# Optimization experiments

Hardware: AMD Instinct MI355X
Metric: run time of the kernel (lower is better)

The kernel has to match this reference:

```python
import jax, jax.numpy as jnp
import numpy as np

N = 100000
E = 1600000
IN_FEATS = 256
OUT_FEATS = 128
THRESHOLD = 0.5


def setup_inputs() -> dict:
    key = jax.random.key(0)
    k1, k2, k3, k4, k5, k6, k7 = jax.random.split(key, 7)
    return {
        "feat": jax.random.normal(k1, (N, IN_FEATS), dtype=jnp.float32),
        "src": jax.random.randint(k2, (E,), 0, N, dtype=jnp.int32),
        "dst": jax.random.randint(k3, (E,), 0, N, dtype=jnp.int32),
        "edge_weight": jax.random.uniform(k4, (E,), dtype=jnp.float32),
        "weight": jax.random.normal(k5, (IN_FEATS, OUT_FEATS), dtype=jnp.float32),
        "bias": jax.random.normal(k6, (OUT_FEATS,), dtype=jnp.float32),
        "mask_real": jax.random.uniform(k7, (IN_FEATS, OUT_FEATS), dtype=jnp.float32),
    }


def reference(feat, src, dst, edge_weight, weight, bias, mask_real):
    ones_e = jnp.ones((E,), dtype=feat.dtype)
    # norm == 'both': scale source feats by out_degree^-0.5 (clamped at 1)
    out_deg = jnp.clip(jax.ops.segment_sum(ones_e, src, num_segments=N), 1.0)
    feat_src = feat * (out_deg ** -0.5)[:, None]  # [N, IN]
    # binarized mask with straight-through estimator (training-mode path)
    hard = (mask_real > THRESHOLD).astype(mask_real.dtype)
    mask_t = jax.lax.stop_gradient(hard - mask_real) + mask_real
    w = mask_t * weight  # [IN, OUT]
    # in_feats > out_feats: project before aggregation
    feat_src = feat_src @ w  # [N, OUT]
    # u_mul_e then sum: gather source feats, scale by edge weight, scatter-add to dst
    msgs = feat_src[src] * edge_weight[:, None]  # [E, OUT]
    rst = jax.ops.segment_sum(msgs, dst, num_segments=N)  # [N, OUT]
    # norm == 'both': scale by in_degree^-0.5 (clamped at 1)
    in_deg = jnp.clip(jax.ops.segment_sum(ones_e, dst, num_segments=N), 1.0)
    rst = rst * (in_deg ** -0.5)[:, None]
    return rst + bias
```

## Files before the change

### kernel.cpp

```cpp
#include <hip/hip_runtime.h>

#define N_NODES 100000
#define N_EDGES 1600000
#define IN_F 256
#define OUT_F 128
#define NBUCK 391
#define NPART 256
#define CHUNK (N_EDGES / NPART)
#define BCAP 5632

#define ODBLK 256
#define ODCHUNK (N_EDGES / ODBLK)
#define ODW 25000

typedef __attribute__((ext_vector_type(8))) short short8;
typedef __attribute__((ext_vector_type(4))) float f32x4;

__device__ __forceinline__ unsigned bf16_rne(float f) {
    unsigned u = __float_as_uint(f);
    return (u + 0x7fffu + ((u >> 16) & 1u)) >> 16;
}

__global__ void mask_w_kernel(const float* __restrict__ weight,
                              const float* __restrict__ mask_real,
                              unsigned short* __restrict__ wmT) {
    int i = blockIdx.x * blockDim.x + threadIdx.x;
    if (i < IN_F * OUT_F) {
        int k = i >> 7;
        int n = i & 127;
        float v = (mask_real[i] > 0.5f) ? weight[i] : 0.0f;
        wmT[(size_t)n * IN_F + k] = (unsigned short)bf16_rne(v);
    }
}

__global__ __launch_bounds__(256) void outdeg_part_kernel(const int* __restrict__ src,
                                                          unsigned* __restrict__ part) {
    __shared__ unsigned h[ODW];
    int b = blockIdx.x, t = threadIdx.x;
    for (int i = t; i < ODW; i += 256) h[i] = 0u;
    __syncthreads();
    int base = b * ODCHUNK;
    for (int i = t; i < ODCHUNK; i += 256) {
        unsigned s = (unsigned)src[base + i];
        atomicAdd(&h[s >> 2], 1u << ((s & 3u) * 8u));
    }
    __syncthreads();
    unsigned* op = part + (size_t)b * ODW;
    for (int i = t; i < ODW; i += 256) op[i] = h[i];
}

__global__ __launch_bounds__(256) void outdeg_reduce_kernel(const unsigned* __restrict__ part,
                                                            unsigned* __restrict__ outpk) {
    int d = blockIdx.x * 256 + threadIdx.x;
    if (d < ODW) {
        unsigned sum = 0u;
#pragma unroll 8
        for (int b = 0; b < ODBLK; b++) sum += part[(size_t)b * ODW + d];
        outpk[d] = sum;
    }
}

__global__ __launch_bounds__(256) void hist_kernel(const int* __restrict__ dst,
                                                   unsigned* __restrict__ hist) {
    __shared__ unsigned h[NBUCK];
    int p = blockIdx.x, t = threadIdx.x;
    for (int b = t; b < NBUCK; b += 256) h[b] = 0u;
    __syncthreads();
    int base = p * CHUNK;
    for (int i = t; i < CHUNK; i += 256)
        atomicAdd(&h[(unsigned)dst[base + i] >> 8], 1u);
    __syncthreads();
    for (int b = t; b < NBUCK; b += 256)
        hist[(size_t)p * NBUCK + b] = h[b];
}

__global__ __launch_bounds__(256) void scan_reduce_hist(const unsigned* __restrict__ hist,
                                                        unsigned* __restrict__ bsum) {
    __shared__ unsigned red[256];
    int b = blockIdx.x, t = threadIdx.x;
    red[t] = hist[(size_t)t * NBUCK + b];
    __syncthreads();
#pragma unroll
    for (int d = 128; d > 0; d >>= 1) {
        if (t < d) red[t] += red[t + d];
        __syncthreads();
    }
    if (t == 0) bsum[b] = red[0];
}

__global__ __launch_bounds__(512) void scan_spine(const unsigned* __restrict__ bsum,
                                                  unsigned* __restrict__ bpref) {
    __shared__ unsigned part[512];
    int t = threadIdx.x;
    unsigned v = (t < NBUCK) ? bsum[t] : 0u;
    part[t] = v;
    __syncthreads();
#pragma unroll
    for (int d = 1; d < 512; d <<= 1) {
        unsigned x = (t >= d) ? part[t - d] : 0u;
        __syncthreads();
        part[t] += x;
        __syncthreads();
    }
    if (t < NBUCK) bpref[t] = part[t] - v;
}

__global__ __launch_bounds__(256) void scan_apply_hist(const unsigned* __restrict__ hist,
                                                       const unsigned* __restrict__ bpref,
                                                       unsigned* __restrict__ scanned) {
    __shared__ unsigned part[256];
    int b = blockIdx.x, t = threadIdx.x;
    unsigned v = hist[(size_t)t * NBUCK + b];
    part[t] = v;
    __syncthreads();
#pragma unroll
    for (int d = 1; d < 256; d <<= 1) {
        unsigned x = (t >= d) ? part[t - d] : 0u;
        __syncthreads();
        part[t] += x;
        __syncthreads();
    }
    scanned[(size_t)b * 256 + t] = bpref[b] + part[t] - v;
}

__global__ __launch_bounds__(256) void scatter_kernel(const int* __restrict__ src,
                                                      const int* __restrict__ dst,
                                                      const float* __restrict__ ew,
                                                      const unsigned* __restrict__ scanned,
                                                      uint2* __restrict__ tmp) {
    __shared__ unsigned cur[NBUCK];
    int p = blockIdx.x, t = threadIdx.x;
    for (int b = t; b < NBUCK; b += 256) cur[b] = scanned[(size_t)b * 256 + p];
    __syncthreads();
    int base = p * CHUNK;
    for (int i = t; i < CHUNK; i += 256) {
        int e = base + i;
        int s = src[e];
        int d = dst[e];
        unsigned pos = atomicAdd(&cur[(unsigned)d >> 8], 1u);
        tmp[pos] = make_uint2((unsigned)s | (((unsigned)d & 255u) << 17),
                              __float_as_uint(ew[e]));
    }
}

__global__ __launch_bounds__(256) void fillB_kernel(const uint2* __restrict__ tmp,
                                                    const unsigned* __restrict__ scanned,
                                                    unsigned* __restrict__ offsets,
                                                    uint2* __restrict__ smeta) {
    __shared__ uint2 ebuf[BCAP];
    __shared__ unsigned hcnt[256];
    __shared__ unsigned pref[256];
    int b = blockIdx.x, t = threadIdx.x;
    unsigned base = scanned[(size_t)b * 256];
    unsigned next = (b == NBUCK - 1) ? (unsigned)N_EDGES : scanned[(size_t)(b + 1) * 256];
    int cnt = (int)(next - base);
    if (cnt > BCAP) cnt = BCAP;
    hcnt[t] = 0u;
    for (int i = t; i < cnt; i += 256) ebuf[i] = tmp[base + i];
    __syncthreads();
    for (int i = t; i < cnt; i += 256) atomicAdd(&hcnt[ebuf[i].x >> 17], 1u);
    __syncthreads();
    unsigned v = hcnt[t];
    pref[t] = v;
    __syncthreads();
#pragma unroll
    for (int d = 1; d < 256; d <<= 1) {
        unsigned x = (t >= d) ? pref[t - d] : 0u;
        __syncthreads();
        pref[t] += x;
        __syncthreads();
    }
    unsigned excl = pref[t] - v;
    int node = b * 256 + t;
    if (node <= N_NODES) offsets[node] = base + excl;
    hcnt[t] = base + excl;
    __syncthreads();
    for (int i = t; i < cnt; i += 256) {
        uint2 m = ebuf[i];
        unsigned pos = atomicAdd(&hcnt[m.x >> 17], 1u);
        smeta[pos] = make_uint2(m.x & 0x1FFFFu, m.y);
    }
}

__global__ __launch_bounds__(256) void gemm_kernel(const float* __restrict__ feat,
                                                   const unsigned short* __restrict__ wmT,
                                                   const unsigned char* __restrict__ outdeg8,
                                                   unsigned short* __restrict__ hb) {
    __shared__ unsigned short sA[64][32];
    __shared__ unsigned short sB[128][40];
    int t = threadIdx.x;
    int row0 = blockIdx.x * 64;
    int lane = t & 63, wv = t >> 6;
    int m16 = lane & 15, quad = lane >> 4;

    f32x4 acc[8];
#pragma unroll
    for (int i = 0; i < 8; i++) acc[i] = (f32x4){0.f, 0.f, 0.f, 0.f};

    int ar = t >> 2;
    int ac = (t & 3) * 8;
    int arow = min(row0 + ar, N_NODES - 1);
    const float* fptr = feat + (size_t)arow * IN_F + ac;
    int bn = t >> 2;
    int bs = (t & 3) * 8;

    for (int k0 = 0; k0 < IN_F; k0 += 32) {
        float4 v0 = *(const float4*)(fptr + k0);
        float4 v1 = *(const float4*)(fptr + k0 + 4);
        uint4 bw0 = *(const uint4*)&wmT[(size_t)bn * IN_F + k0 + bs];
        uint4 bw1 = *(const uint4*)&wmT[(size_t)(bn + 64) * IN_F + k0 + bs];
        uint4 pk;
        pk.x = bf16_rne(v0.x) | (bf16_rne(v0.y) << 16);
        pk.y = bf16_rne(v0.z) | (bf16_rne(v0.w) << 16);
        pk.z = bf16_rne(v1.x) | (bf16_rne(v1.y) << 16);
        pk.w = bf16_rne(v1.z) | (bf16_rne(v1.w) << 16);
        __syncthreads();
        *(uint4*)&sA[ar][ac] = pk;
        *(uint4*)&sB[bn][bs] = bw0;
        *(uint4*)&sB[bn + 64][bs] = bw1;
        __syncthreads();
        short8 a = *(const short8*)&sA[wv * 16 + m16][quad * 8];
#pragma unroll
        for (int nt = 0; nt < 8; nt++) {
            short8 b = *(const short8*)&sB[nt * 16 + m16][quad * 8];
            acc[nt] = __builtin_amdgcn_mfma_f32_16x16x32_bf16(a, b, acc[nt], 0, 0, 0);
        }
    }
#pragma unroll
    for (int reg = 0; reg < 4; reg++) {
        int row = row0 + wv * 16 + quad * 4 + reg;
        if (row < N_NODES) {
            float s = rsqrtf(fmaxf((float)outdeg8[row], 1.0f));
#pragma unroll
            for (int nt = 0; nt < 8; nt++)
                hb[(size_t)row * OUT_F + nt * 16 + m16] =
                    (unsigned short)bf16_rne(acc[nt][reg] * s);
        }
    }
}

__global__ __launch_bounds__(256) void gather_kernel(const uint2* __restrict__ smeta,
                                                     const unsigned* __restrict__ offsets,
                                                     const uint4* __restrict__ hrows4,
                                                     const float* __restrict__ bias,
                                                     float* __restrict__ out) {
    int lane = threadIdx.x & 63;
    int n = blockIdx.x * 4 + (threadIdx.x >> 6);
    int g = lane >> 4;
    int q = lane & 15;
    unsigned beg = offsets[n], end = offsets[n + 1];
    int deg = (int)(end - beg);

    float acc[8];
#pragma unroll
    for (int i = 0; i < 8; i++) acc[i] = 0.0f;

    for (int base = 0; base < deg; base += 64) {
        int c = min(64, deg - base);
        unsigned sv = 0u;
        float wv = 0.0f;
        if (lane < c) {
            uint2 m = smeta[beg + base + lane];
            sv = m.x;
            wv = __uint_as_float(m.y);
        }
        int nch = (c + 3) >> 2;
#pragma unroll 4
        for (int j = 0; j < nch; j++) {
            int ei = (j << 2) + g;
            unsigned s = __shfl(sv, ei);
            float w = __shfl(wv, ei);
            uint4 h = hrows4[(size_t)s * 16u + q];
            acc[0] = fmaf(__uint_as_float(h.x << 16), w, acc[0]);
            acc[1] = fmaf(__uint_as_float(h.x & 0xffff0000u), w, acc[1]);
            acc[2] = fmaf(__uint_as_float(h.y << 16), w, acc[2]);
            acc[3] = fmaf(__uint_as_float(h.y & 0xffff0000u), w, acc[3]);
            acc[4] = fmaf(__uint_as_float(h.z << 16), w, acc[4]);
            acc[5] = fmaf(__uint_as_float(h.z & 0xffff0000u), w, acc[5]);
            acc[6] = fmaf(__uint_as_float(h.w << 16), w, acc[6]);
            acc[7] = fmaf(__uint_as_float(h.w & 0xffff0000u), w, acc[7]);
        }
    }

#pragma unroll
    for (int i = 0; i < 8; i++) {
        acc[i] += __shfl_xor(acc[i], 16);
        acc[i] += __shfl_xor(acc[i], 32);
    }

    float o0, o1;
    if (g == 0)      { o0 = acc[0]; o1 = acc[1]; }
    else if (g == 1) { o0 = acc[2]; o1 = acc[3]; }
    else if (g == 2) { o0 = acc[4]; o1 = acc[5]; }
    else             { o0 = acc[6]; o1 = acc[7]; }

    float sc = rsqrtf(fmaxf((float)deg, 1.0f));
    int col = q * 8 + g * 2;
    float2 b = *(const float2*)&bias[col];
    float2 o = make_float2(o0 * sc + b.x, o1 * sc + b.y);
    *(float2*)&out[(size_t)n * OUT_F + col] = o;
}

extern "C" void kernel_launch(void* const* d_in, const int* in_sizes, int n_in,
                              void* d_out, int out_size, void* d_ws, size_t ws_size,
                              hipStream_t stream) {
    const float* feat      = (const float*)d_in[0];
    const int*   src       = (const int*)d_in[1];
    const int*   dst       = (const int*)d_in[2];
    const float* ew        = (const float*)d_in[3];
    const float* weight    = (const float*)d_in[4];
    const float* bias      = (const float*)d_in[5];
    const float* mask_real = (const float*)d_in[6];
    float* out = (float*)d_out;

    char* ws = (char*)d_ws;
    size_t o = 0;
    auto take = [&](size_t bytes) {
        char* p = ws + o;
        o = (o + bytes + 255) & ~(size_t)255;
        return p;
    };
    unsigned short* wmT     = (unsigned short*)take((size_t)IN_F * OUT_F * 2);
    unsigned*       outpk   = (unsigned*)take((size_t)ODW * 4);
    unsigned*       offs    = (unsigned*)take((size_t)(N_NODES + 1) * 4);
    unsigned*       hist    = (unsigned*)take((size_t)NPART * NBUCK * 4);
    unsigned*       scanned = (unsigned*)take((size_t)NBUCK * 256 * 4);
    unsigned*       bsum    = (unsigned*)take((size_t)NBUCK * 4);
    unsigned*       bpref   = (unsigned*)take((size_t)NBUCK * 4);
    uint2*          tmp     = (uint2*)take((size_t)N_EDGES * 8);
    uint2*          smeta   = (uint2*)take((size_t)N_EDGES * 8);
    unsigned short* hrows   = (unsigned short*)take((size_t)N_NODES * OUT_F * 2);

    unsigned* odpart = (unsigned*)tmp;

    mask_w_kernel<<<(IN_F * OUT_F + 255) / 256, 256, 0, stream>>>(weight, mask_real, wmT);
    outdeg_part_kernel<<<ODBLK, 256, 0, stream>>>(src, odpart);
    outdeg_reduce_kernel<<<(ODW + 255) / 256, 256, 0, stream>>>(odpart, outpk);
    hist_kernel<<<NPART, 256, 0, stream>>>(dst, hist);
    scan_reduce_hist<<<NBUCK, 256, 0, stream>>>(hist, bsum);
    scan_spine<<<1, 512, 0, stream>>>(bsum, bpref);
    scan_apply_hist<<<NBUCK, 256, 0, stream>>>(hist, bpref, scanned);
    scatter_kernel<<<NPART, 256, 0, stream>>>(src, dst, ew, scanned, tmp);
    gemm_kernel<<<(N_NODES + 63) / 64, 256, 0, stream>>>(feat, wmT,
                                                         (const unsigned char*)outpk, hrows);
    fillB_kernel<<<NBUCK, 256, 0, stream>>>(tmp, scanned, offs, smeta);
    gather_kernel<<<N_NODES / 4, 256, 0, stream>>>(smeta, offs,
                                                   (const uint4*)hrows, bias, out);
}
```

Baseline: 350.7 us.

## Pack edge metadata into one word and hoist full weight tile into LDS

Edge source index (17 bits) and edge weight truncated to 15 high bits are packed into one 32-bit word, halving the sorted edge metadata written by fillB and read by gather, and removing one shuffle per edge. The GEMM now loads the whole masked weight matrix into padded shared memory once per block and feeds A fragments directly from registers, eliminating per-k-step barriers and A-tile shared-memory staging. The packing lowers edge weight precision to about 7 mantissa bits with rounding, and the larger LDS footprint may reduce GEMM occupancy.

New measurement: 358.5 us. +2.2%, slower.

```diff
diff --git a/kernel.cpp b/kernel.cpp
--- a/kernel.cpp
+++ b/kernel.cpp
@@ -146,7 +146,7 @@
 __global__ __launch_bounds__(256) void fillB_kernel(const uint2* __restrict__ tmp,
                                                     const unsigned* __restrict__ scanned,
                                                     unsigned* __restrict__ offsets,
-                                                    uint2* __restrict__ smeta) {
+                                                    unsigned* __restrict__ smeta) {
     __shared__ uint2 ebuf[BCAP];
     __shared__ unsigned hcnt[256];
     __shared__ unsigned pref[256];
@@ -178,7 +178,7 @@
     for (int i = t; i < cnt; i += 256) {
         uint2 m = ebuf[i];
         unsigned pos = atomicAdd(&hcnt[m.x >> 17], 1u);
-        smeta[pos] = make_uint2(m.x & 0x1FFFFu, m.y);
+        smeta[pos] = ((m.y + 0x10000u) & 0xFFFE0000u) | (m.x & 0x1FFFFu);
     }
 }
 
@@ -186,43 +186,39 @@
                                                    const unsigned short* __restrict__ wmT,
                                                    const unsigned char* __restrict__ outdeg8,
                                                    unsigned short* __restrict__ hb) {
-    __shared__ unsigned short sA[64][32];
-    __shared__ unsigned short sB[128][40];
+    __shared__ unsigned short sB[128][264];
     int t = threadIdx.x;
-    int row0 = blockIdx.x * 64;
+    for (int idx = t; idx < (128 * 256 / 8); idx += 256) {
+        int flat = idx * 8;
+        int n = flat >> 8, k = flat & 255;
+        *(uint4*)&sB[n][k] = *(const uint4*)&wmT[flat];
+    }
+    __syncthreads();
+
     int lane = t & 63, wv = t >> 6;
     int m16 = lane & 15, quad = lane >> 4;
+    int row0 = blockIdx.x * 64;
+    int arow = min(row0 + wv * 16 + m16, N_NODES - 1);
+    const float* fp = feat + (size_t)arow * IN_F + quad * 8;
 
     f32x4 acc[8];
 #pragma unroll
     for (int i = 0; i < 8; i++) acc[i] = (f32x4){0.f, 0.f, 0.f, 0.f};
 
-    int ar = t >> 2;
-    int ac = (t & 3) * 8;
-    int arow = min(row0 + ar, N_NODES - 1);
-    const float* fptr = feat + (size_t)arow * IN_F + ac;
-    int bn = t >> 2;
-    int bs = (t & 3) * 8;
-
+#pragma unroll
     for (int k0 = 0; k0 < IN_F; k0 += 32) {
-        float4 v0 = *(const float4*)(fptr + k0);
-        float4 v1 = *(const float4*)(fptr + k0 + 4);
-        uint4 bw0 = *(const uint4*)&wmT[(size_t)bn * IN_F + k0 + bs];
-        uint4 bw1 = *(const uint4*)&wmT[(size_t)(bn + 64) * IN_F + k0 + bs];
+        float4 v0 = *(const float4*)(fp + k0);
+        float4 v1 = *(const float4*)(fp + k0 + 4);
         uint4 pk;
         pk.x = bf16_rne(v0.x) | (bf16_rne(v0.y) << 16);
         pk.y = bf16_rne(v0.z) | (bf16_rne(v0.w) << 16);
         pk.z = bf16_rne(v1.x) | (bf16_rne(v1.y) << 16);
         pk.w = bf16_rne(v1.z) | (bf16_rne(v1.w) << 16);
-        __syncthreads();
-        *(uint4*)&sA[ar][ac] = pk;
-        *(uint4*)&sB[bn][bs] = bw0;
-        *(uint4*)&sB[bn + 64][bs] = bw1;
-        __syncthreads();
-        short8 a = *(const short8*)&sA[wv * 16 + m16][quad * 8];
+        short8 a;
+        *(uint4*)&a = pk;
 #pragma unroll
         for (int nt = 0; nt < 8; nt++) {
-            short8 b = *(const short8*)&sB[nt * 16 + m16][quad * 8];
+            short8 b = *(const short8*)&sB[nt * 16 + m16][k0 + quad * 8];
             acc[nt] = __builtin_amdgcn_mfma_f32_16x16x32_bf16(a, b, acc[nt], 0, 0, 0);
         }
     }
@@ -239,7 +235,7 @@
     }
 }
 
-__global__ __launch_bounds__(256) void gather_kernel(const uint2* __restrict__ smeta,
+__global__ __launch_bounds__(256) void gather_kernel(const unsigned* __restrict__ smeta,
                                                      const unsigned* __restrict__ offsets,
                                                      const uint4* __restrict__ hrows4,
                                                      const float* __restrict__ bias,
@@ -257,19 +253,15 @@
 
     for (int base = 0; base < deg; base += 64) {
         int c = min(64, deg - base);
-        unsigned sv = 0u;
-        float wv = 0.0f;
-        if (lane < c) {
-            uint2 m = smeta[beg + base + lane];
-            sv = m.x;
-            wv = __uint_as_float(m.y);
-        }
+        unsigned pv = 0u;
+        if (lane < c) pv = smeta[beg + base + lane];
         int nch = (c + 3) >> 2;
 #pragma unroll 4
         for (int j = 0; j < nch; j++) {
             int ei = (j << 2) + g;
-            unsigned s = __shfl(sv, ei);
-            float w = __shfl(wv, ei);
+            unsigned p = __shfl(pv, ei);
+            unsigned s = p & 0x1FFFFu;
+            float w = __uint_as_float(p & 0xFFFE0000u);
             uint4 h = hrows4[(size_t)s * 16u + q];
             acc[0] = fmaf(__uint_as_float(h.x << 16), w, acc[0]);
             acc[1] = fmaf(__uint_as_float(h.x & 0xffff0000u), w, acc[1]);
@@ -328,7 +320,7 @@
     unsigned*       bsum    = (unsigned*)take((size_t)NBUCK * 4);
     unsigned*       bpref   = (unsigned*)take((size_t)NBUCK * 4);
     uint2*          tmp     = (uint2*)take((size_t)N_EDGES * 8);
-    uint2*          smeta   = (uint2*)take((size_t)N_EDGES * 8);
+    unsigned*       smeta   = (unsigned*)take((size_t)N_EDGES * 4);
     unsigned short* hrows   = (unsigned short*)take((size_t)N_NODES * OUT_F * 2);
 
     unsigned* odpart = (unsigned*)tmp;
```
